# Kernel optimization log

Measured on AMD Instinct MI355X. Metric: run time of the kernel, lower is better.

Reference implementation:

```python
import jax, jax.numpy as jnp
import numpy as np
from jax import lax

B, C, O, K, H, W = 8, 16, 16, 3, 512, 512
STRIDE, PAD = 1, 1
BN_EPS = 1e-5


def setup_inputs() -> dict:
    key = jax.random.key(0)
    ks = jax.random.split(key, 5)
    # kaiming_normal fan_out for a (O, I, K, K, K) tensor: fan_out = O * K**3
    std = float(np.sqrt(2.0 / (O * K ** 3)))
    return {
        "x": jax.random.normal(ks[0], (B, C, H, W), jnp.float32),
        "w_fft_real": jax.random.normal(ks[1], (O, C, K, K, K), jnp.float32) * std,
        "w_fft_imag": jax.random.normal(ks[2], (O, C, K, K, K), jnp.float32) * std,
        "rot_w": jax.random.normal(ks[3], (3, C), jnp.float32) * float(np.sqrt(1.0 / C)),
        "rot_b": jnp.zeros((3,), jnp.float32),
        "bn_gamma": jnp.ones((3,), jnp.float32),
        "bn_beta": jnp.zeros((3,), jnp.float32),
    }


def _forward(x, w_fft_real, w_fft_imag, rot_w, rot_b, bn_gamma, bn_beta):
    # --- rotation params: 1x1 conv -> BatchNorm2d (training-mode batch stats) ---
    z = jnp.einsum("bchw,oc->bohw", x, rot_w) + rot_b[None, :, None, None]  # (B,3,H,W)
    mu = jnp.mean(z, axis=(0, 2, 3), keepdims=True)
    var = jnp.mean((z - mu) ** 2, axis=(0, 2, 3), keepdims=True)  # biased, as torch BN
    z = (z - mu) * lax.rsqrt(var + BN_EPS)
    z = z * bn_gamma[None, :, None, None] + bn_beta[None, :, None, None]
    angles = jnp.mean(z, axis=(2, 3))            # (B,3)
    angle = jnp.sum(angles, axis=1, keepdims=True)  # (B,1)
    angle = jnp.tanh(angle) * (jnp.pi / 4)
    cos_theta = jnp.cos(angle)[:, 0]             # (B,)

    # --- FFT-domain phase rotation of the 3D kernel ---
    freq = jnp.fft.fftfreq(K).astype(jnp.float32)
    fx, fy, fz = jnp.meshgrid(freq, freq, freq, indexing="ij")
    fsum = fx + fy + fz                           # (K,K,K)
    phase = jnp.exp(-2j * jnp.pi * (cos_theta[:, None, None, None] * fsum))  # (B,K,K,K) complex
    w_fft = (w_fft_real + 1j * w_fft_imag)        # (O,C,K,K,K)
    w_rot = w_fft[None] * phase[:, None, None]    # (B,O,C,K,K,K)
    rotated = jnp.fft.ifftn(w_rot, axes=(-3, -2, -1)).real

    # --- take middle depth slice -> per-sample 2D kernels ---
    mid = K // 2
    w2d = rotated[:, :, :, mid, :, :]             # (B,O,C,K,K)
    gw = w2d.reshape(B * O, C, K, K)

    # --- batch-as-groups conv2d ---
    xg = x.reshape(1, B * C, H, W)
    out = lax.conv_general_dilated(
        xg, gw,
        window_strides=(STRIDE, STRIDE),
        padding=[(PAD, PAD), (PAD, PAD)],
        feature_group_count=B,
        dimension_numbers=("NCHW", "OIHW", "NCHW"),
    )
    return out.reshape(B, O, out.shape[2], out.shape[3])


def reference(x, w_fft_real, w_fft_imag, rot_w, rot_b, bn_gamma, bn_beta):
    return _forward(x, w_fft_real, w_fft_imag, rot_w, rot_b, bn_gamma, bn_beta)
```

## Files before the change

kernel.cpp:

```cpp
#include <hip/hip_runtime.h>

#define HW 262144
#define CIN 16
#define OUTC 16

#define WS_PARTIALS 0
#define WS_COS      12288
#define WS_WB_F     12296

typedef float  floatx4 __attribute__((ext_vector_type(4)));
typedef short  bf16x8  __attribute__((ext_vector_type(8)));

__device__ __forceinline__ ushort bf16_rne(float f) {
  unsigned u = __float_as_uint(f);
  unsigned r = (u + 0x7FFFu + ((u >> 16) & 1u)) >> 16;
  return (ushort)r;
}
__device__ __forceinline__ void bf16_split(float f, ushort& hi, ushort& lo) {
  hi = bf16_rne(f);
  float fh = __uint_as_float(((unsigned)hi) << 16);
  lo = bf16_rne(f - fh);
}

__global__ __launch_bounds__(256) void k_reduce(const float* __restrict__ x,
                                                const float* __restrict__ rot_w,
                                                const float* __restrict__ rot_b,
                                                float* __restrict__ partials) {
  const int blk = blockIdx.x;
  const int b = blk >> 8;
  const int s = blk & 255;
  const int t = threadIdx.x;

  float rw[3][16];
#pragma unroll
  for (int k = 0; k < 3; k++)
#pragma unroll
    for (int c = 0; c < 16; c++) rw[k][c] = rot_w[k * 16 + c];
  float rb[3];
#pragma unroll
  for (int k = 0; k < 3; k++) rb[k] = rot_b[k];

  const float* xb = x + (size_t)b * CIN * HW + s * 1024 + t * 4;

  float z[3][4];
#pragma unroll
  for (int k = 0; k < 3; k++)
#pragma unroll
    for (int j = 0; j < 4; j++) z[k][j] = 0.f;

#pragma unroll
  for (int c = 0; c < 16; c++) {
    float4 v = *reinterpret_cast<const float4*>(xb + (size_t)c * HW);
#pragma unroll
    for (int k = 0; k < 3; k++) {
      z[k][0] += rw[k][c] * v.x;
      z[k][1] += rw[k][c] * v.y;
      z[k][2] += rw[k][c] * v.z;
      z[k][3] += rw[k][c] * v.w;
    }
  }

  float vals[6];
#pragma unroll
  for (int k = 0; k < 3; k++) {
    float sz = 0.f, sz2 = 0.f;
#pragma unroll
    for (int j = 0; j < 4; j++) {
      float zz = z[k][j] + rb[k];
      sz += zz;
      sz2 += zz * zz;
    }
    vals[k] = sz;
    vals[3 + k] = sz2;
  }

  __shared__ float redsh[4][6];
  const int wave = t >> 6, lane = t & 63;
#pragma unroll
  for (int v = 0; v < 6; v++) {
    float val = vals[v];
#pragma unroll
    for (int off = 32; off; off >>= 1) val += __shfl_down(val, off, 64);
    if (lane == 0) redsh[wave][v] = val;
  }
  __syncthreads();
  if (t < 6)
    partials[blk * 6 + t] = redsh[0][t] + redsh[1][t] + redsh[2][t] + redsh[3][t];
}

__global__ __launch_bounds__(256) void k_stats(const float* __restrict__ partials,
                                               const float* __restrict__ bn_gamma,
                                               const float* __restrict__ bn_beta,
                                               float* __restrict__ cos_theta) {
  __shared__ float Msh[8][3];
  __shared__ float varsum[3];
  const int t = threadIdx.x;

  if (t < 24) {
    int b = t / 3, c = t - b * 3;
    float s = 0.f;
    for (int i = 0; i < 256; i++) s += partials[(b * 256 + i) * 6 + c];
    Msh[b][c] = s;
  }
  if (t >= 64) {
    int c = (t - 64) >> 6;
    int lane = t & 63;
    float s = 0.f;
    for (int i = lane; i < 2048; i += 64) s += partials[i * 6 + 3 + c];
#pragma unroll
    for (int off = 32; off; off >>= 1) s += __shfl_down(s, off, 64);
    if (lane == 0) varsum[c] = s;
  }
  __syncthreads();

  if (t < 8) {
    const float invN = 1.0f / (8.0f * 262144.0f);
    const float invHW = 1.0f / 262144.0f;
    float angle = 0.f;
#pragma unroll
    for (int c = 0; c < 3; c++) {
      float tot = 0.f;
#pragma unroll
      for (int b = 0; b < 8; b++) tot += Msh[b][c];
      float mu = tot * invN;
      float var = varsum[c] * invN - mu * mu;
      float rs = rsqrtf(var + 1e-5f);
      angle += (Msh[t][c] * invHW - mu) * rs * bn_gamma[c] + bn_beta[c];
    }
    float a = tanhf(angle) * 0.7853981633974483f;
    cos_theta[t] = cosf(a);
  }
}

__global__ __launch_bounds__(256) void k_rotw(const float* __restrict__ wfr,
                                              const float* __restrict__ wfi,
                                              const float* __restrict__ cos_theta,
                                              ushort* __restrict__ wB) {
  const int b = blockIdx.x;
  const int t = threadIdx.x;
  const int o = t & 15;
  const int c = t >> 4;

  const float ct = cos_theta[b];
  const float phi = ct * 2.0943951023931953f;
  float sp, cp;
  sincosf(phi, &sp, &cp);
  const float ur[3] = {1.f, cp, cp};
  const float ui[3] = {0.f, -sp, sp};
  const float wr3[3] = {1.f, -0.5f, -0.5f};
  const float wi3[3] = {0.f, 0.8660254037844386f, -0.8660254037844386f};

  float cr[3][3], ci[3][3];
#pragma unroll
  for (int k = 0; k < 3; k++)
#pragma unroll
    for (int m = 0; m < 3; m++) {
      int e = (k * m) % 3;
      cr[k][m] = ur[k] * wr3[e] - ui[k] * wi3[e];
      ci[k][m] = ur[k] * wi3[e] + ui[k] * wr3[e];
    }

  const float* Ar = wfr + (o * 16 + c) * 27;
  const float* Ai = wfi + (o * 16 + c) * 27;

  float outv[9];
#pragma unroll
  for (int i = 0; i < 9; i++) outv[i] = 0.f;

#pragma unroll
  for (int k1 = 0; k1 < 3; k1++) {
    float ar[9], ai[9];
#pragma unroll
    for (int i = 0; i < 9; i++) { ar[i] = Ar[k1 * 9 + i]; ai[i] = Ai[k1 * 9 + i]; }
    float hr[3][3], hi2[3][3];
#pragma unroll
    for (int k2 = 0; k2 < 3; k2++)
#pragma unroll
      for (int q = 0; q < 3; q++) {
        float sr = 0.f, si = 0.f;
#pragma unroll
        for (int k3 = 0; k3 < 3; k3++) {
          float xr = ar[k2 * 3 + k3], xi = ai[k2 * 3 + k3];
          sr += xr * cr[k3][q] - xi * ci[k3][q];
          si += xr * ci[k3][q] + xi * cr[k3][q];
        }
        hr[k2][q] = sr;
        hi2[k2][q] = si;
      }
    float drr = cr[k1][1], dii = ci[k1][1];
#pragma unroll
    for (int p = 0; p < 3; p++)
#pragma unroll
      for (int q = 0; q < 3; q++) {
        float sr = 0.f, si = 0.f;
#pragma unroll
        for (int k2 = 0; k2 < 3; k2++) {
          sr += hr[k2][q] * cr[k2][p] - hi2[k2][q] * ci[k2][p];
          si += hr[k2][q] * ci[k2][p] + hi2[k2][q] * cr[k2][p];
        }
        outv[p * 3 + q] += sr * drr - si * dii;
      }
  }

#pragma unroll
  for (int tap = 0; tap < 9; tap++) {
    float v = outv[tap] * (1.0f / 27.0f);
    int k = tap * 16 + c;
    int kb = k >> 5;
    int g = (k >> 3) & 3;
    int j = k & 7;
    int ln = g * 16 + o;
    ushort hi, lo;
    bf16_split(v, hi, lo);
    int idx = ((b * 5 + kb) * 2) * 512 + ln * 8 + j;
    wB[idx] = hi;
    wB[idx + 512] = lo;
  }

#pragma unroll
  for (int u = 0; u < 2; u++) {
    int e = t * 2 + u;
    int hl = e >> 8;
    int rem = e & 255;
    int kk = 144 + (rem >> 4);
    int o2 = rem & 15;
    int g2 = (kk >> 3) & 3;
    int ln2 = g2 * 16 + o2;
    int j2 = kk & 7;
    wB[((b * 5 + 4) * 2 + hl) * 512 + ln2 * 8 + j2] = 0;
  }
}

__global__ __launch_bounds__(256, 4) void k_conv(const float* __restrict__ x,
                                                 const ushort* __restrict__ wB,
                                                 float* __restrict__ out) {
  __shared__ ushort xsb[18 * 1096];

  const int id = blockIdx.x;
  const int nid = (id & 7) * 512 + (id >> 3);
  const int b = nid >> 9;
  const int rem0 = nid & 511;
  const int row0 = (rem0 >> 4) * 16;
  const int col0 = (rem0 & 15) * 32;
  const int t = threadIdx.x;
  const int lane = t & 63;

  const ushort* wBb = wB + b * 5120;
  bf16x8 wh[5], wl[5];
#pragma unroll
  for (int kb = 0; kb < 5; kb++) {
    wh[kb] = *reinterpret_cast<const bf16x8*>(wBb + (kb * 2 + 0) * 512 + lane * 8);
    wl[kb] = *reinterpret_cast<const bf16x8*>(wBb + (kb * 2 + 1) * 512 + lane * 8);
  }

  const float* xb = x + (size_t)b * CIN * HW;
#pragma unroll
  for (int it = 0; it < 5; it++) {
    int p = it * 256 + t;
    if (p < 1224) {
      int row = p / 68;
      int rem2 = p - row * 68;
      int col = rem2 >> 1;
      int chalf = rem2 & 1;
      int gr = row0 - 1 + row;
      int gc = col0 - 1 + col;
      bool ok = ((unsigned)gr < 512u) && ((unsigned)gc < 512u);
      const float* src = xb + (size_t)(chalf * 8) * HW + gr * 512 + gc;
      bf16x8 hv, lv;
#pragma unroll
      for (int j = 0; j < 8; j++) {
        float v = ok ? src[(size_t)j * HW] : 0.f;
        ushort hi, lo;
        bf16_split(v, hi, lo);
        hv[j] = (short)hi;
        lv[j] = (short)lo;
      }
      int swz = (col >> 1) & 3;
      int base = row * 1096 + col * 32;
      *reinterpret_cast<bf16x8*>(&xsb[base + ((chalf ^ swz) << 3)]) = hv;
      *reinterpret_cast<bf16x8*>(&xsb[base + (((2 | chalf) ^ swz) << 3)]) = lv;
    }
  }

  const int m = lane & 15;
  const int g = lane >> 4;
  const int chalf = g & 1;
  const int tsel = g >> 1;
  int offh[5], offl[5];
#pragma unroll
  for (int kb = 0; kb < 5; kb++) {
    int tap = kb * 2 + tsel;
    if (tap > 8) tap = 8;
    int dy = tap / 3;
    int dx = tap - dy * 3;
    int mdx = m + dx;
    int swz = (mdx >> 1) & 3;
    offh[kb] = dy * 1096 + mdx * 32 + ((chalf ^ swz) << 3);
    offl[kb] = dy * 1096 + mdx * 32 + (((2 | chalf) ^ swz) << 3);
  }

  __syncthreads();

  const int w = t >> 6;
  const int oo = lane & 15;
  const int quad = lane >> 4;
#pragma unroll
  for (int s = 0; s < 8; s++) {
    int r = w * 4 + (s >> 1);
    int cg = s & 1;
    int base = r * 1096 + cg * 512;
    floatx4 acc = {0.f, 0.f, 0.f, 0.f};
#pragma unroll
    for (int kb = 0; kb < 5; kb++) {
      bf16x8 a_hi = *reinterpret_cast<const bf16x8*>(&xsb[base + offh[kb]]);
      bf16x8 a_lo = *reinterpret_cast<const bf16x8*>(&xsb[base + offl[kb]]);
      acc = __builtin_amdgcn_mfma_f32_16x16x32_bf16(a_hi, wh[kb], acc, 0, 0, 0);
      acc = __builtin_amdgcn_mfma_f32_16x16x32_bf16(a_hi, wl[kb], acc, 0, 0, 0);
      acc = __builtin_amdgcn_mfma_f32_16x16x32_bf16(a_lo, wh[kb], acc, 0, 0, 0);
    }
    float* dst = out + (size_t)(b * OUTC + oo) * HW + (size_t)(row0 + r) * 512 +
                 col0 + cg * 16 + quad * 4;
    *reinterpret_cast<float4*>(dst) = make_float4(acc[0], acc[1], acc[2], acc[3]);
  }
}

extern "C" void kernel_launch(void* const* d_in, const int* in_sizes, int n_in,
                              void* d_out, int out_size, void* d_ws, size_t ws_size,
                              hipStream_t stream) {
  const float* x      = (const float*)d_in[0];
  const float* wfr    = (const float*)d_in[1];
  const float* wfi    = (const float*)d_in[2];
  const float* rot_w  = (const float*)d_in[3];
  const float* rot_b  = (const float*)d_in[4];
  const float* bn_g   = (const float*)d_in[5];
  const float* bn_b   = (const float*)d_in[6];
  float* out = (float*)d_out;
  float* ws  = (float*)d_ws;

  float* partials = ws + WS_PARTIALS;
  float* cosw     = ws + WS_COS;
  ushort* wB      = (ushort*)(ws + WS_WB_F);

  k_reduce<<<2048, 256, 0, stream>>>(x, rot_w, rot_b, partials);
  k_stats<<<1, 256, 0, stream>>>(partials, bn_g, bn_b, cosw);
  k_rotw<<<8, 256, 0, stream>>>(wfr, wfi, cosw, wB);
  k_conv<<<4096, 256, 0, stream>>>(x, wB, out);
}
```

Before: 296.2 us.

## Fuse reduce, stats, weight rotation and conv into one cooperative persistent kernel

Replaces four separate launches with a single cooperative kernel of 1024 blocks that uses grid-wide syncs between the BN-statistics reduction, the per-batch kernel rotation and the bf16-split MFMA convolution. Each block processes two reduce strips and four conv tiles, so launch gaps and tail effects between stages go away and the stats and rotation stages are folded in. Conv output now uses nontemporal stores. In exchange it needs co-residency of all blocks (launch_bounds 256,4), pays two grid barriers, and falls back to the old path if the cooperative launch fails.

```diff
diff --git a/kernel.cpp b/kernel.cpp
--- a/kernel.cpp
+++ b/kernel.cpp
@@ -1,4 +1,6 @@
 #include <hip/hip_runtime.h>
+#include <hip/hip_cooperative_groups.h>
+namespace cg = cooperative_groups;
 
 #define HW 262144
 #define CIN 16
@@ -20,6 +22,308 @@
   hi = bf16_rne(f);
   float fh = __uint_as_float(((unsigned)hi) << 16);
   lo = bf16_rne(f - fh);
+}
+
+__global__ __launch_bounds__(256, 4) void k_fused(
+    const float* __restrict__ x, const float* __restrict__ wfr,
+    const float* __restrict__ wfi, const float* __restrict__ rot_w,
+    const float* __restrict__ rot_b, const float* __restrict__ bn_g,
+    const float* __restrict__ bn_b, float* __restrict__ out,
+    float* __restrict__ ws) {
+  __shared__ __align__(16) char smem[18 * 1096 * 2];
+
+  float* partials = ws + WS_PARTIALS;
+  ushort* wB = (ushort*)(ws + WS_WB_F);
+
+  const int blk = blockIdx.x;
+  const int t = threadIdx.x;
+  const int lane = t & 63;
+
+  {
+    float rw[3][16];
+#pragma unroll
+    for (int k = 0; k < 3; k++)
+#pragma unroll
+      for (int c = 0; c < 16; c++) rw[k][c] = rot_w[k * 16 + c];
+    float rb[3];
+#pragma unroll
+    for (int k = 0; k < 3; k++) rb[k] = rot_b[k];
+
+    float* redsh = (float*)smem;
+    const int wave = t >> 6;
+
+    for (int ss = 0; ss < 2; ss++) {
+      const int strip = blk * 2 + ss;
+      const int b = strip >> 8;
+      const int s = strip & 255;
+      const float* xb = x + (size_t)b * CIN * HW + s * 1024 + t * 4;
+
+      float z[3][4];
+#pragma unroll
+      for (int k = 0; k < 3; k++)
+#pragma unroll
+        for (int j = 0; j < 4; j++) z[k][j] = 0.f;
+
+#pragma unroll
+      for (int c = 0; c < 16; c++) {
+        float4 v = *reinterpret_cast<const float4*>(xb + (size_t)c * HW);
+#pragma unroll
+        for (int k = 0; k < 3; k++) {
+          z[k][0] += rw[k][c] * v.x;
+          z[k][1] += rw[k][c] * v.y;
+          z[k][2] += rw[k][c] * v.z;
+          z[k][3] += rw[k][c] * v.w;
+        }
+      }
+
+      float vals[6];
+#pragma unroll
+      for (int k = 0; k < 3; k++) {
+        float sz = 0.f, sz2 = 0.f;
+#pragma unroll
+        for (int j = 0; j < 4; j++) {
+          float zz = z[k][j] + rb[k];
+          sz += zz;
+          sz2 += zz * zz;
+        }
+        vals[k] = sz;
+        vals[3 + k] = sz2;
+      }
+
+#pragma unroll
+      for (int v = 0; v < 6; v++) {
+        float val = vals[v];
+#pragma unroll
+        for (int off = 32; off; off >>= 1) val += __shfl_down(val, off, 64);
+        if (lane == 0) redsh[wave * 6 + v] = val;
+      }
+      __syncthreads();
+      if (t < 6)
+        partials[strip * 6 + t] =
+            redsh[0 * 6 + t] + redsh[1 * 6 + t] + redsh[2 * 6 + t] + redsh[3 * 6 + t];
+      __syncthreads();
+    }
+  }
+
+  cg::this_grid().sync();
+
+  if (blk < 8) {
+    float* Msh = (float*)smem;
+    float* vsum = Msh + 24;
+
+    if (t < 24) {
+      int b = t / 3, c = t - b * 3;
+      float s = 0.f;
+      for (int i = 0; i < 256; i++) s += partials[(b * 256 + i) * 6 + c];
+      Msh[b * 3 + c] = s;
+    }
+    if (t >= 64) {
+      int c = (t - 64) >> 6;
+      int ln = t & 63;
+      float s = 0.f;
+      for (int i = ln; i < 2048; i += 64) s += partials[i * 6 + 3 + c];
+#pragma unroll
+      for (int off = 32; off; off >>= 1) s += __shfl_down(s, off, 64);
+      if (ln == 0) vsum[c] = s;
+    }
+    __syncthreads();
+
+    const float invN = 1.0f / (8.0f * 262144.0f);
+    const float invHW = 1.0f / 262144.0f;
+    float angle = 0.f;
+#pragma unroll
+    for (int c = 0; c < 3; c++) {
+      float tot = 0.f;
+#pragma unroll
+      for (int b = 0; b < 8; b++) tot += Msh[b * 3 + c];
+      float mu = tot * invN;
+      float var = vsum[c] * invN - mu * mu;
+      float rs = rsqrtf(var + 1e-5f);
+      angle += (Msh[blk * 3 + c] * invHW - mu) * rs * bn_g[c] + bn_b[c];
+    }
+    const float ct = cosf(tanhf(angle) * 0.7853981633974483f);
+
+    const int o = t & 15;
+    const int c = t >> 4;
+    const float phi = ct * 2.0943951023931953f;
+    float sp, cp;
+    sincosf(phi, &sp, &cp);
+    const float ur[3] = {1.f, cp, cp};
+    const float ui[3] = {0.f, -sp, sp};
+    const float wr3[3] = {1.f, -0.5f, -0.5f};
+    const float wi3[3] = {0.f, 0.8660254037844386f, -0.8660254037844386f};
+
+    float cr[3][3], ci[3][3];
+#pragma unroll
+    for (int k = 0; k < 3; k++)
+#pragma unroll
+      for (int m2 = 0; m2 < 3; m2++) {
+        int e = (k * m2) % 3;
+        cr[k][m2] = ur[k] * wr3[e] - ui[k] * wi3[e];
+        ci[k][m2] = ur[k] * wi3[e] + ui[k] * wr3[e];
+      }
+
+    const float* Ar = wfr + (o * 16 + c) * 27;
+    const float* Ai = wfi + (o * 16 + c) * 27;
+
+    float outv[9];
+#pragma unroll
+    for (int i = 0; i < 9; i++) outv[i] = 0.f;
+
+#pragma unroll
+    for (int k1 = 0; k1 < 3; k1++) {
+      float ar[9], ai[9];
+#pragma unroll
+      for (int i = 0; i < 9; i++) { ar[i] = Ar[k1 * 9 + i]; ai[i] = Ai[k1 * 9 + i]; }
+      float hr[3][3], hi2[3][3];
+#pragma unroll
+      for (int k2 = 0; k2 < 3; k2++)
+#pragma unroll
+        for (int q = 0; q < 3; q++) {
+          float sr = 0.f, si = 0.f;
+#pragma unroll
+          for (int k3 = 0; k3 < 3; k3++) {
+            float xr = ar[k2 * 3 + k3], xi = ai[k2 * 3 + k3];
+            sr += xr * cr[k3][q] - xi * ci[k3][q];
+            si += xr * ci[k3][q] + xi * cr[k3][q];
+          }
+          hr[k2][q] = sr;
+          hi2[k2][q] = si;
+        }
+      float drr = cr[k1][1], dii = ci[k1][1];
+#pragma unroll
+      for (int p = 0; p < 3; p++)
+#pragma unroll
+        for (int q = 0; q < 3; q++) {
+          float sr = 0.f, si = 0.f;
+#pragma unroll
+          for (int k2 = 0; k2 < 3; k2++) {
+            sr += hr[k2][q] * cr[k2][p] - hi2[k2][q] * ci[k2][p];
+            si += hr[k2][q] * ci[k2][p] + hi2[k2][q] * cr[k2][p];
+          }
+          outv[p * 3 + q] += sr * drr - si * dii;
+        }
+    }
+
+#pragma unroll
+    for (int tap = 0; tap < 9; tap++) {
+      float v = outv[tap] * (1.0f / 27.0f);
+      int k = tap * 16 + c;
+      int kb = k >> 5;
+      int g = (k >> 3) & 3;
+      int j = k & 7;
+      int ln = g * 16 + o;
+      ushort hi, lo;
+      bf16_split(v, hi, lo);
+      int idx = ((blk * 5 + kb) * 2) * 512 + ln * 8 + j;
+      wB[idx] = hi;
+      wB[idx + 512] = lo;
+    }
+#pragma unroll
+    for (int u = 0; u < 2; u++) {
+      int e = t * 2 + u;
+      int hl = e >> 8;
+      int rem = e & 255;
+      int kk = 144 + (rem >> 4);
+      int o2 = rem & 15;
+      int g2 = (kk >> 3) & 3;
+      int ln2 = g2 * 16 + o2;
+      int j2 = kk & 7;
+      wB[((blk * 5 + 4) * 2 + hl) * 512 + ln2 * 8 + j2] = 0;
+    }
+  }
+
+  cg::this_grid().sync();
+
+  {
+    ushort* xsb = (ushort*)smem;
+    const int b = blk & 7;
+    const ushort* wBb = wB + b * 5120;
+    bf16x8 wh[5], wl[5];
+#pragma unroll
+    for (int kb = 0; kb < 5; kb++) {
+      wh[kb] = *reinterpret_cast<const bf16x8*>(wBb + (kb * 2 + 0) * 512 + lane * 8);
+      wl[kb] = *reinterpret_cast<const bf16x8*>(wBb + (kb * 2 + 1) * 512 + lane * 8);
+    }
+
+    const int m = lane & 15;
+    const int g = lane >> 4;
+    const int chalf = g & 1;
+    const int tsel = g >> 1;
+    int offh[5], offl[5];
+#pragma unroll
+    for (int kb = 0; kb < 5; kb++) {
+      int tap = kb * 2 + tsel;
+      if (tap > 8) tap = 8;
+      int dy = tap / 3;
+      int dx = tap - dy * 3;
+      int mdx = m + dx;
+      int swz = (mdx >> 1) & 3;
+      offh[kb] = dy * 1096 + mdx * 32 + ((chalf ^ swz) << 3);
+      offl[kb] = dy * 1096 + mdx * 32 + (((2 | chalf) ^ swz) << 3);
+    }
+
+    const float* xb = x + (size_t)b * CIN * HW;
+    const int w = t >> 6;
+    const int oo = lane & 15;
+    const int quad = lane >> 4;
+
+    for (int tt = 0; tt < 4; tt++) {
+      const int rem0 = (blk >> 3) * 4 + tt;
+      const int row0 = (rem0 >> 4) * 16;
+      const int col0 = (rem0 & 15) * 32;
+
+      __syncthreads();
+
+#pragma unroll
+      for (int it = 0; it < 5; it++) {
+        int p = it * 256 + t;
+        if (p < 1224) {
+          int row = p / 68;
+          int rem2 = p - row * 68;
+          int col = rem2 >> 1;
+          int ch = rem2 & 1;
+          int gr = row0 - 1 + row;
+          int gc = col0 - 1 + col;
+          bool ok = ((unsigned)gr < 512u) && ((unsigned)gc < 512u);
+          const float* src = xb + (size_t)(ch * 8) * HW + gr * 512 + gc;
+          bf16x8 hv, lv;
+#pragma unroll
+          for (int j = 0; j < 8; j++) {
+            float v = ok ? src[(size_t)j * HW] : 0.f;
+            ushort hi, lo;
+            bf16_split(v, hi, lo);
+            hv[j] = (short)hi;
+            lv[j] = (short)lo;
+          }
+          int swz = (col >> 1) & 3;
+          int base = row * 1096 + col * 32;
+          *reinterpret_cast<bf16x8*>(&xsb[base + ((ch ^ swz) << 3)]) = hv;
+          *reinterpret_cast<bf16x8*>(&xsb[base + (((2 | ch) ^ swz) << 3)]) = lv;
+        }
+      }
+      __syncthreads();
+
+#pragma unroll
+      for (int s = 0; s < 8; s++) {
+        int r = w * 4 + (s >> 1);
+        int cg2 = s & 1;
+        int base = r * 1096 + cg2 * 512;
+        floatx4 acc = {0.f, 0.f, 0.f, 0.f};
+#pragma unroll
+        for (int kb = 0; kb < 5; kb++) {
+          bf16x8 a_hi = *reinterpret_cast<const bf16x8*>(&xsb[base + offh[kb]]);
+          bf16x8 a_lo = *reinterpret_cast<const bf16x8*>(&xsb[base + offl[kb]]);
+          acc = __builtin_amdgcn_mfma_f32_16x16x32_bf16(a_hi, wh[kb], acc, 0, 0, 0);
+          acc = __builtin_amdgcn_mfma_f32_16x16x32_bf16(a_hi, wl[kb], acc, 0, 0, 0);
+          acc = __builtin_amdgcn_mfma_f32_16x16x32_bf16(a_lo, wh[kb], acc, 0, 0, 0);
+        }
+        float* dst = out + (size_t)(b * OUTC + oo) * HW +
+                     (size_t)(row0 + r) * 512 + col0 + cg2 * 16 + quad * 4;
+        __builtin_nontemporal_store(acc, reinterpret_cast<floatx4*>(dst));
+      }
+    }
+  }
 }
 
 __global__ __launch_bounds__(256) void k_reduce(const float* __restrict__ x,
@@ -337,12 +641,18 @@
   float* out = (float*)d_out;
   float* ws  = (float*)d_ws;
 
-  float* partials = ws + WS_PARTIALS;
-  float* cosw     = ws + WS_COS;
-  ushort* wB      = (ushort*)(ws + WS_WB_F);
-
-  k_reduce<<<2048, 256, 0, stream>>>(x, rot_w, rot_b, partials);
-  k_stats<<<1, 256, 0, stream>>>(partials, bn_g, bn_b, cosw);
-  k_rotw<<<8, 256, 0, stream>>>(wfr, wfi, cosw, wB);
-  k_conv<<<4096, 256, 0, stream>>>(x, wB, out);
-}
+  void* args[] = {(void*)&x, (void*)&wfr, (void*)&wfi, (void*)&rot_w,
+                  (void*)&rot_b, (void*)&bn_g, (void*)&bn_b, (void*)&out,
+                  (void*)&ws};
+  hipError_t err = hipLaunchCooperativeKernel((void*)k_fused, dim3(1024),
+                                              dim3(256), args, 0, stream);
+  if (err != hipSuccess) {
+    float* partials = ws + WS_PARTIALS;
+    float* cosw     = ws + WS_COS;
+    ushort* wB      = (ushort*)(ws + WS_WB_F);
+    k_reduce<<<2048, 256, 0, stream>>>(x, rot_w, rot_b, partials);
+    k_stats<<<1, 256, 0, stream>>>(partials, bn_g, bn_b, cosw);
+    k_rotw<<<8, 256, 0, stream>>>(wfr, wfi, cosw, wB);
+    k_conv<<<4096, 256, 0, stream>>>(x, wB, out);
+  }
+}
```

New measurement: 552.5 us. 1.87x slower.
